# Kernel optimization log

Hardware: AMD Instinct MI355X
Metric: run time of the kernel (lower is better)

## Reference

```python
import jax, jax.numpy as jnp
import numpy as np
from functools import partial

K = 3
P = K * K * K          # 27 kernel points
G = 2                  # groups
PAD = 1
STRIDE = 1
DIL = 1
AXIS_SCALE = (0.5, 1.0, 1.0)   # (x, y, z) offset axis scale
CUR_SCALE = 0.5                # warmup scale at global_step=0
EPS = 1e-5


def setup_inputs() -> dict:
    key = jax.random.key(0)
    ks = jax.random.split(key, 8)
    C, OC = 64, 64
    N, D, H, W = 1, 32, 32, 32
    inp = {
        "x": jax.random.normal(ks[0], (N, C, D, H, W), jnp.float32),
        "dw_w": jax.random.normal(ks[1], (C, 1, K, K, K), jnp.float32) * 0.1,
        "gn_w": jnp.ones((C,), jnp.float32),
        "gn_b": jnp.zeros((C,), jnp.float32),
        "inp_w": jax.random.normal(ks[2], (C, C), jnp.float32) * (1.0 / np.sqrt(C)),
        "inp_b": jnp.zeros((C,), jnp.float32),
        # offset/mask weights are zero-init in the module; use small random values
        # so the deformable sampling path is exercised nontrivially.
        "off_w": jax.random.normal(ks[3], (C, G * P * 3), jnp.float32) * 0.01,
        "off_b": jnp.zeros((G * P * 3,), jnp.float32),
        "mask_w": jax.random.normal(ks[4], (C, G * P), jnp.float32) * 0.01,
        "mask_b": jnp.tile(jnp.full((P,), -5.0, jnp.float32).at[P // 2].set(0.0), (G,)),
        "out_w": jax.random.normal(ks[5], (C, OC), jnp.float32) * (1.0 / np.sqrt(C)),
        "out_b": jnp.zeros((OC,), jnp.float32),
    }
    return inp


def _trilinear(vol, loc):
    # vol: [Dp, Hp, Wp, gc]; loc: [..., 3] with (x, y, z) in [-1, 1]
    # grid_sample semantics: align_corners=False, padding_mode='zeros'
    Dp, Hp, Wp, _ = vol.shape
    ix = (loc[..., 0] + 1.0) * 0.5 * Wp - 0.5
    iy = (loc[..., 1] + 1.0) * 0.5 * Hp - 0.5
    iz = (loc[..., 2] + 1.0) * 0.5 * Dp - 0.5
    x0f, y0f, z0f = jnp.floor(ix), jnp.floor(iy), jnp.floor(iz)
    fx, fy, fz = ix - x0f, iy - y0f, iz - z0f
    x0, y0, z0 = x0f.astype(jnp.int32), y0f.astype(jnp.int32), z0f.astype(jnp.int32)
    out = jnp.zeros(loc.shape[:-1] + (vol.shape[-1],), vol.dtype)
    for dz in (0, 1):
        wz = fz if dz else 1.0 - fz
        cz = z0 + dz
        for dy in (0, 1):
            wy = fy if dy else 1.0 - fy
            cy = y0 + dy
            for dx in (0, 1):
                wx = fx if dx else 1.0 - fx
                cx = x0 + dx
                valid = ((cz >= 0) & (cz < Dp) & (cy >= 0) & (cy < Hp)
                         & (cx >= 0) & (cx < Wp))
                v = vol[jnp.clip(cz, 0, Dp - 1),
                        jnp.clip(cy, 0, Hp - 1),
                        jnp.clip(cx, 0, Wp - 1)]  # [..., gc]
                out = out + (wz * wy * wx * valid.astype(vol.dtype))[..., None] * v
    return out


def _forward(x, dw_w, gn_w, gn_b, inp_w, inp_b, off_w, off_b,
             mask_w, mask_b, out_w, out_b):
    N, C, D, H, W = x.shape
    gc = C // G
    # --- dw_conv: depthwise conv3d + GroupNorm(1, C) + GELU ---
    xc = jax.lax.conv_general_dilated(
        x, dw_w, window_strides=(1, 1, 1), padding=[(PAD, PAD)] * 3,
        dimension_numbers=("NCDHW", "OIDHW", "NCDHW"), feature_group_count=C)
    mu = xc.mean(axis=(1, 2, 3, 4), keepdims=True)
    var = ((xc - mu) ** 2).mean(axis=(1, 2, 3, 4), keepdims=True)
    xn = (xc - mu) * jax.lax.rsqrt(var + EPS)
    xn = xn * gn_w[None, :, None, None, None] + gn_b[None, :, None, None, None]
    x1 = jnp.transpose(jax.nn.gelu(xn), (0, 2, 3, 4, 1))       # [N,D,H,W,C]
    # --- offset / mask / input projection ---
    offset = x1 @ off_w + off_b                                  # [N,D,H,W,G*P*3]
    mask = jax.nn.softmax(
        (x1 @ mask_w + mask_b).reshape(N, D, H, W, G, P), axis=-1)
    xp = jnp.transpose(x, (0, 2, 3, 4, 1)) @ inp_w + inp_b       # [N,D,H,W,C]
    # --- core deformable sampling ---
    x_pad = jnp.pad(xp, ((0, 0), (PAD, PAD), (PAD, PAD), (PAD, PAD), (0, 0)))
    Dp, Hp, Wp = D + 2 * PAD, H + 2 * PAD, W + 2 * PAD
    Do = (D + 2 * PAD - DIL * (K - 1) - 1) // STRIDE + 1
    Ho = (H + 2 * PAD - DIL * (K - 1) - 1) // STRIDE + 1
    Wo = (W + 2 * PAD - DIL * (K - 1) - 1) // STRIDE + 1
    # reference grid (x/Wp, y/Hp, z/Dp)
    zc, yc, xc_ = jnp.meshgrid(jnp.arange(Do, dtype=jnp.float32),
                               jnp.arange(Ho, dtype=jnp.float32),
                               jnp.arange(Wo, dtype=jnp.float32), indexing="ij")
    ref = jnp.stack(((xc_ * STRIDE + PAD + 0.5) / Wp,
                     (yc * STRIDE + PAD + 0.5) / Hp,
                     (zc * STRIDE + PAD + 0.5) / Dp), axis=-1)   # [Do,Ho,Wo,3]
    # kernel grid
    lin = jnp.linspace(-(K - 1) // 2, (K - 1) // 2, K, dtype=jnp.float32)
    kz, ky, kx = jnp.meshgrid(lin, lin, lin, indexing="ij")
    kgrid = jnp.stack((kx * DIL / Wp, ky * DIL / Hp, kz * DIL / Dp),
                      axis=-1).reshape(P, 3)
    off = offset.reshape(N, Do, Ho, Wo, G, P, 3)
    off_norm = off / jnp.array([Wp, Hp, Dp], jnp.float32)
    axis = jnp.array(AXIS_SCALE, jnp.float32)
    loc = (ref[None, :, :, :, None, None, :]
           + kgrid[None, None, None, None, None, :, :]
           + off_norm * axis * CUR_SCALE)
    loc = loc * 2.0 - 1.0                                        # [N,Do,Ho,Wo,G,P,3]
    vol = jnp.transpose(x_pad.reshape(N, Dp, Hp, Wp, G, gc),
                        (0, 4, 1, 2, 3, 5))                      # [N,G,Dp,Hp,Wp,gc]
    locs = jnp.transpose(loc, (0, 4, 1, 2, 3, 5, 6))             # [N,G,Do,Ho,Wo,P,3]
    sampled = jax.vmap(jax.vmap(_trilinear))(vol, locs)          # [N,G,Do,Ho,Wo,P,gc]
    out = jnp.einsum("ngdhwpc,ndhwgp->ndhwgc", sampled, mask)
    out = out.reshape(N, Do, Ho, Wo, C)
    return out @ out_w + out_b                                   # [N,Do,Ho,Wo,OC]


def reference(x, dw_w, gn_w, gn_b, inp_w, inp_b, off_w, off_b,
              mask_w, mask_b, out_w, out_b):
    return _forward(x, dw_w, gn_w, gn_b, inp_w, inp_b, off_w, off_b,
                    mask_w, mask_b, out_w, out_b)
```

## Files before the change

kernel.cpp:

```cpp
#include <hip/hip_runtime.h>
#include <hip/hip_fp16.h>
#include <math.h>

#define SP 32768
#define PW 38
#define PW2 (PW*PW)
#define PVOX (PW*PW*PW)
#define OMS 228

typedef short bf16x8 __attribute__((ext_vector_type(8)));
typedef unsigned short u16x4 __attribute__((ext_vector_type(4)));
typedef float f32x4 __attribute__((ext_vector_type(4)));

__device__ __forceinline__ unsigned short f2b(float f) {
    unsigned u = __float_as_uint(f);
    u = (u + 0x7FFFu + ((u >> 16) & 1u)) >> 16;
    return (unsigned short)u;
}
__device__ __forceinline__ float b2f1(unsigned short s) {
    return __uint_as_float(((unsigned)s) << 16);
}
__device__ __forceinline__ __half2 h2(unsigned u) {
    return *reinterpret_cast<__half2*>(&u);
}
__device__ __forceinline__ int vox_of(int sb, int v) {
    int tw = sb & 7, th = (sb >> 3) & 15, td = sb >> 7;
    int vw = v & 3, vh = (v >> 2) & 1, vd = v >> 3;
    return (((td << 1) + vd) << 10) + (((th << 1) + vh) << 5) + (tw << 2) + vw;
}

__global__ void k_front(const float* __restrict__ x, const float* __restrict__ dw,
                        const float* __restrict__ off_w, const float* __restrict__ mask_w,
                        const float* __restrict__ off_b, const float* __restrict__ mask_b,
                        const float* __restrict__ inp_w, const float* __restrict__ inp_b,
                        const float* __restrict__ out_w,
                        unsigned short* __restrict__ WcatB, float* __restrict__ bcat,
                        unsigned short* __restrict__ outB,
                        unsigned short* __restrict__ xcb, float* __restrict__ partials,
                        unsigned short* __restrict__ xpad) {
    int bb = blockIdx.x, tid = threadIdx.x;
    if (bb < 72) {
        int idx = bb * 256 + tid;
        int j = idx >> 6, k = idx & 63;
        if (j < 224) {
            float v = 0.f;
            if (j < 162) v = off_w[k * 162 + j];
            else if (j < 216) v = mask_w[k * 54 + (j - 162)];
            WcatB[j * 64 + k] = f2b(v);
            if (k == 0) bcat[j] = (j < 162) ? off_b[j] : (j < 216 ? mask_b[j - 162] : 0.f);
        } else {
            outB[(j - 224) * 64 + k] = f2b(out_w[k * 64 + (j - 224)]);
        }
        return;
    }
    if (bb < 2120) {
        int b4 = bb - 72;
        int e4 = b4 * 256 + tid;
        int c = e4 >> 13, s4 = (e4 & 8191) << 2;
        int d = s4 >> 10, h = (s4 >> 5) & 31, w0 = s4 & 31;
        const float* xs = x + (size_t)c * SP;
        const float* wt = dw + c * 27;
        float a0 = 0.f, a1 = 0.f, a2 = 0.f, a3 = 0.f;
#pragma unroll
        for (int kd = 0; kd < 3; ++kd) {
            int zz = d + kd - 1; if ((unsigned)zz >= 32u) continue;
#pragma unroll
            for (int kh = 0; kh < 3; ++kh) {
                int yy = h + kh - 1; if ((unsigned)yy >= 32u) continue;
                const float* row = xs + (zz << 10) + (yy << 5) + w0;
                float4 L = *(const float4*)row;
                float xl = (w0 > 0) ? row[-1] : 0.f;
                float xr = (w0 < 28) ? row[4] : 0.f;
                const float* wr = wt + kd * 9 + kh * 3;
                float wm = wr[0], wc = wr[1], wp = wr[2];
                a0 = __builtin_fmaf(wm, xl,  __builtin_fmaf(wc, L.x, __builtin_fmaf(wp, L.y, a0)));
                a1 = __builtin_fmaf(wm, L.x, __builtin_fmaf(wc, L.y, __builtin_fmaf(wp, L.z, a1)));
                a2 = __builtin_fmaf(wm, L.y, __builtin_fmaf(wc, L.z, __builtin_fmaf(wp, L.w, a2)));
                a3 = __builtin_fmaf(wm, L.z, __builtin_fmaf(wc, L.w, __builtin_fmaf(wp, xr,  a3)));
            }
        }
        u16x4 o4; o4[0] = f2b(a0); o4[1] = f2b(a1); o4[2] = f2b(a2); o4[3] = f2b(a3);
        *(u16x4*)(xcb + (size_t)e4 * 4) = o4;
        float s1 = a0 + a1 + a2 + a3;
        float s2 = a0 * a0 + a1 * a1 + a2 * a2 + a3 * a3;
#pragma unroll
        for (int off = 32; off > 0; off >>= 1) {
            s1 += __shfl_xor(s1, off);
            s2 += __shfl_xor(s2, off);
        }
        __shared__ float ws[8];
        int wv = tid >> 6, lane = tid & 63;
        if (lane == 0) { ws[wv * 2] = s1; ws[wv * 2 + 1] = s2; }
        __syncthreads();
        if (tid == 0) {
            partials[b4 * 2 + 0] = ws[0] + ws[2] + ws[4] + ws[6];
            partials[b4 * 2 + 1] = ws[1] + ws[3] + ws[5] + ws[7];
        }
        return;
    }
    if (bb < 2632) {
        __shared__ unsigned short tileT[64][72];
        __shared__ unsigned short tileB[64][72];
        int s0b = (bb - 2120) * 64;
        int row = tid >> 6, lane = tid & 63;
        for (int c = row; c < 64; c += 4)
            tileT[lane][c] = f2b(x[(size_t)c * SP + s0b + lane]);
        {
            int n = tid & 63, k0 = (tid >> 6) * 16;
            u16x4 wb[4];
#pragma unroll
            for (int i = 0; i < 16; ++i)
                wb[i >> 2][i & 3] = f2b(inp_w[(size_t)(k0 + i) * 64 + n]);
#pragma unroll
            for (int q = 0; q < 4; ++q)
                *(u16x4*)(&tileB[n][k0 + q * 4]) = wb[q];
        }
        __syncthreads();
        int wv = row, quad = lane >> 4, col = lane & 15;
        int s0 = s0b + wv * 16;
        bf16x8 a0 = *(const bf16x8*)(&tileT[wv * 16 + col][quad * 8]);
        bf16x8 a1 = *(const bf16x8*)(&tileT[wv * 16 + col][32 + quad * 8]);
        int vp[4];
#pragma unroll
        for (int r = 0; r < 4; ++r) {
            int s = s0 + (quad << 2) + r;
            vp[r] = (((s >> 10) + 2) * PW + ((s >> 5) & 31) + 2) * PW + (s & 31) + 2;
        }
#pragma unroll
        for (int nt = 0; nt < 4; ++nt) {
            int n0 = nt * 16;
            bf16x8 b0 = *(const bf16x8*)(&tileB[n0 + col][quad * 8]);
            bf16x8 b1 = *(const bf16x8*)(&tileB[n0 + col][32 + quad * 8]);
            f32x4 c = {0.f, 0.f, 0.f, 0.f};
            c = __builtin_amdgcn_mfma_f32_16x16x32_bf16(a0, b0, c, 0, 0, 0);
            c = __builtin_amdgcn_mfma_f32_16x16x32_bf16(a1, b1, c, 0, 0, 0);
            float bq = inp_b[n0 + col];
#pragma unroll
            for (int r = 0; r < 4; ++r)
                xpad[(size_t)vp[r] * 64 + n0 + col] =
                    __half_as_ushort(__float2half(c[r] + bq));
        }
        return;
    }
    int cblk = bb - 2632;
    int j = tid >> 4, c4 = tid & 15;
    u16x4 z = {0, 0, 0, 0};
#pragma unroll
    for (int k = 0; k < 4; ++k) {
        int v = cblk * 64 + k * 16 + j;
        if (v >= PVOX) break;
        int zz = v / PW2, r = v - zz * PW2, yy = r / PW, xx = r - yy * PW;
        if (zz < 2 || zz > 33 || yy < 2 || yy > 33 || xx < 2 || xx > 33)
            *(u16x4*)(xpad + (size_t)v * 64 + c4 * 4) = z;
    }
}

template<int P0, int NP>
__device__ __forceinline__ void sampleN(const float* __restrict__ orow,
                                        const float* __restrict__ mrow,
                                        const char* __restrict__ volc,
                                        float xb, float yb, float zb,
                                        float* __restrict__ acc) {
#pragma unroll
    for (int i = 0; i < NP; ++i) {
        const int p = P0 + i;
        const int px = p % 3, py = (p / 3) % 3, pz = p / 9;
        float ox = orow[p * 3 + 0], oy = orow[p * 3 + 1], oz = orow[p * 3 + 2];
        float mk = mrow[p];
        float ix = __builtin_fmaf(0.25f, ox, xb + (float)px);
        float iy = __builtin_fmaf(0.5f, oy, yb + (float)py);
        float iz = __builtin_fmaf(0.5f, oz, zb + (float)pz);
        ix = fminf(fmaxf(ix, 0.f), 36.f);
        iy = fminf(fmaxf(iy, 0.f), 36.f);
        iz = fminf(fmaxf(iz, 0.f), 36.f);
        float xf = floorf(ix), yf = floorf(iy), zf = floorf(iz);
        float fx = ix - xf, fy = iy - yf, fz = iz - zf;
        float fi = __builtin_fmaf(zf, (float)PW2, __builtin_fmaf(yf, (float)PW, xf));
        int ib = ((int)fi) << 7;
        const char* base = volc + ib;
        uint4 r000 = *(const uint4*)(base);
        uint4 r001 = *(const uint4*)(base + 128);
        uint4 r010 = *(const uint4*)(base + PW * 128);
        uint4 r011 = *(const uint4*)(base + PW * 128 + 128);
        uint4 r100 = *(const uint4*)(base + PW2 * 128);
        uint4 r101 = *(const uint4*)(base + PW2 * 128 + 128);
        uint4 r110 = *(const uint4*)(base + (PW2 + PW) * 128);
        uint4 r111 = *(const uint4*)(base + (PW2 + PW) * 128 + 128);
        __half2 fx2 = __float2half2_rn(fx);
        __half2 fy2 = __float2half2_rn(fy);
        __half2 fz2 = __float2half2_rn(fz);
        #define TRI(comp, ci)                                                   \
        {                                                                       \
            __half2 t0 = __hfma2(fx2, __hsub2(h2(r001.comp), h2(r000.comp)), h2(r000.comp)); \
            __half2 t1 = __hfma2(fx2, __hsub2(h2(r011.comp), h2(r010.comp)), h2(r010.comp)); \
            __half2 t2 = __hfma2(fx2, __hsub2(h2(r101.comp), h2(r100.comp)), h2(r100.comp)); \
            __half2 t3 = __hfma2(fx2, __hsub2(h2(r111.comp), h2(r110.comp)), h2(r110.comp)); \
            __half2 u0 = __hfma2(fy2, __hsub2(t1, t0), t0);                     \
            __half2 u1 = __hfma2(fy2, __hsub2(t3, t2), t2);                     \
            __half2 rr = __hfma2(fz2, __hsub2(u1, u0), u0);                     \
            float2 ff = __half22float2(rr);                                     \
            acc[2 * ci + 0] = __builtin_fmaf(mk, ff.x, acc[2 * ci + 0]);        \
            acc[2 * ci + 1] = __builtin_fmaf(mk, ff.y, acc[2 * ci + 1]);        \
        }
        TRI(x, 0) TRI(y, 1) TRI(z, 2) TRI(w, 3)
        #undef TRI
    }
}

template<int P0, int NP>
__device__ __forceinline__ void sampleL(const float* __restrict__ orow,
                                        const float* __restrict__ mrow,
                                        const char* __restrict__ volp,
                                        float xb, float yb, float zb,
                                        float* __restrict__ acc) {
    float ox[NP], oy[NP], oz[NP], mk[NP];
#pragma unroll
    for (int i = 0; i < NP; ++i) {
        ox[i] = orow[(P0 + i) * 3 + 0];
        oy[i] = orow[(P0 + i) * 3 + 1];
        oz[i] = orow[(P0 + i) * 3 + 2];
        mk[i] = mrow[P0 + i];
    }
#pragma unroll
    for (int i = 0; i < NP; ++i) {
        const int p = P0 + i;
        const int px = p % 3, py = (p / 3) % 3, pz = p / 9;
        float ix = __builtin_fmaf(0.25f, ox[i], xb + (float)px);
        float iy = __builtin_fmaf(0.5f, oy[i], yb + (float)py);
        float iz = __builtin_fmaf(0.5f, oz[i], zb + (float)pz);
        ix = fminf(fmaxf(ix, 0.f), 6.999f);
        iy = fminf(fmaxf(iy, 0.f), 4.999f);
        iz = fminf(fmaxf(iz, 0.f), 4.999f);
        float xf = floorf(ix), yf = floorf(iy), zf = floorf(iz);
        float fx = ix - xf, fy = iy - yf, fz = iz - zf;
        float fi = __builtin_fmaf(zf, 48.f, __builtin_fmaf(yf, 8.f, xf));
        int rr = (int)fi;
        #define RD(o) (*(const uint4*)(volp + ((rr + (o)) << 7)))
        uint4 r000 = RD(0);
        uint4 r001 = RD(1);
        uint4 r010 = RD(8);
        uint4 r011 = RD(9);
        uint4 r100 = RD(48);
        uint4 r101 = RD(49);
        uint4 r110 = RD(56);
        uint4 r111 = RD(57);
        #undef RD
        __half2 fx2 = __float2half2_rn(fx);
        __half2 fy2 = __float2half2_rn(fy);
        __half2 fz2 = __float2half2_rn(fz);
        float m = mk[i];
        #define TRI(comp, ci)                                                   \
        {                                                                       \
            __half2 t0 = __hfma2(fx2, __hsub2(h2(r001.comp), h2(r000.comp)), h2(r000.comp)); \
            __half2 t1 = __hfma2(fx2, __hsub2(h2(r011.comp), h2(r010.comp)), h2(r010.comp)); \
            __half2 t2 = __hfma2(fx2, __hsub2(h2(r101.comp), h2(r100.comp)), h2(r100.comp)); \
            __half2 t3 = __hfma2(fx2, __hsub2(h2(r111.comp), h2(r110.comp)), h2(r110.comp)); \
            __half2 u0 = __hfma2(fy2, __hsub2(t1, t0), t0);                     \
            __half2 u1 = __hfma2(fy2, __hsub2(t3, t2), t2);                     \
            __half2 rr2 = __hfma2(fz2, __hsub2(u1, u0), u0);                    \
            float2 ff = __half22float2(rr2);                                    \
            acc[2 * ci + 0] = __builtin_fmaf(m, ff.x, acc[2 * ci + 0]);         \
            acc[2 * ci + 1] = __builtin_fmaf(m, ff.y, acc[2 * ci + 1]);         \
        }
        TRI(x, 0) TRI(y, 1) TRI(z, 2) TRI(w, 3)
        #undef TRI
    }
}

__global__ void __launch_bounds__(256, 2) k_main(const unsigned short* __restrict__ xcb,
                                                 const float* __restrict__ partials,
                                                 const float* __restrict__ gn_w,
                                                 const float* __restrict__ gn_b,
                                                 const unsigned short* __restrict__ xpad,
                                                 const unsigned short* __restrict__ WcatB,
                                                 const float* __restrict__ bcat,
                                                 const unsigned short* __restrict__ outB,
                                                 const float* __restrict__ out_b,
                                                 float* __restrict__ out) {
    __shared__ float om_s[16 * OMS];
    __shared__ unsigned short smb[16 * 72];
    __shared__ char vol[288 * 128];
    __shared__ float pbuf[16 * 64];
    __shared__ float gnw_s[64], gnb_s[64], ws[8];
    int tid = threadIdx.x, wv = tid >> 6, lane = tid & 63;
    int quad = lane >> 4, col = lane & 15;
    int sb = ((blockIdx.x & 7) << 8) | (blockIdx.x >> 3);
    int tw = sb & 7, th = (sb >> 3) & 15, td = sb >> 7;
    {
        const char* xp = (const char*)xpad;
#pragma unroll
        for (int k = 0; k < 3; ++k) {
            uint4 t[3];
#pragma unroll
            for (int j = 0; j < 3; ++j) {
                int u = tid + (k * 3 + j) * 256;
                int rr = u >> 3, ch = u & 7;
                int dz = rr / 48, rem = rr - dz * 48, dy = rem >> 3, dx = rem & 7;
                int pv = ((2 * td + dz) * PW + (2 * th + dy)) * PW + 4 * tw + dx;
                t[j] = *(const uint4*)(xp + ((size_t)pv << 7) + (ch << 4));
            }
#pragma unroll
            for (int j = 0; j < 3; ++j) {
                int u = tid + (k * 3 + j) * 256;
                *(uint4*)(vol + (u << 4)) = t[j];
            }
        }
    }
    {
        if (tid < 64) { gnw_s[tid] = gn_w[tid]; gnb_s[tid] = gn_b[tid]; }
        float a = 0.f, b = 0.f;
#pragma unroll
        for (int i = 0; i < 4; ++i) {
            float4 t = *(const float4*)(partials + 4 * (tid + i * 256));
            a += t.x + t.z;
            b += t.y + t.w;
        }
#pragma unroll
        for (int off = 32; off > 0; off >>= 1) {
            a += __shfl_xor(a, off);
            b += __shfl_xor(b, off);
        }
        if (lane == 0) { ws[wv * 2] = a; ws[wv * 2 + 1] = b; }
    }
    __syncthreads();
    const float Minv = 1.f / 2097152.f;
    float mu = (ws[0] + ws[2] + ws[4] + ws[6]) * Minv;
    float var = (ws[1] + ws[3] + ws[5] + ws[7]) * Minv - mu * mu;
    float rsq = rsqrtf(var + 1e-5f);
    {
        int v = tid >> 4, c0 = (tid & 15) * 4;
        int sv = vox_of(sb, v);
        u16x4 av;
#pragma unroll
        for (int i = 0; i < 4; ++i) {
            int c = c0 + i;
            float vx = (b2f1(xcb[(size_t)c * SP + sv]) - mu) * rsq * gnw_s[c] + gnb_s[c];
            float t2 = 1.5957691216057308f * (vx + 0.044715f * vx * vx * vx);
            av[i] = f2b(vx / (1.f + __expf(-t2)));
        }
        *(u16x4*)(&smb[v * 72 + c0]) = av;
    }
    __syncthreads();
    {
        bf16x8 a0 = *(const bf16x8*)(&smb[col * 72 + quad * 8]);
        bf16x8 a1 = *(const bf16x8*)(&smb[col * 72 + 32 + quad * 8]);
        for (int jt = wv; jt < 14; jt += 4) {
            int n0 = jt * 16;
            bf16x8 b0 = *(const bf16x8*)(WcatB + (n0 + col) * 64 + quad * 8);
            bf16x8 b1 = *(const bf16x8*)(WcatB + (n0 + col) * 64 + 32 + quad * 8);
            f32x4 c = {0.f, 0.f, 0.f, 0.f};
            c = __builtin_amdgcn_mfma_f32_16x16x32_bf16(a0, b0, c, 0, 0, 0);
            c = __builtin_amdgcn_mfma_f32_16x16x32_bf16(a1, b1, c, 0, 0, 0);
            float bb = bcat[n0 + col];
            int n = n0 + col, slot;
            if (n < 162) slot = n + ((n >= 81) ? 3 : 0);
            else { int n2 = n - 162; slot = 168 + n2 + ((n2 >= 27) ? 1 : 0); }
            if (n < 216) {
#pragma unroll
                for (int r = 0; r < 4; ++r)
                    om_s[(quad * 4 + r) * OMS + slot] = c[r] + bb;
            }
        }
    }
    __syncthreads();
    {
        int row = lane >> 2, sub = lane & 3;
        int vloc = (wv & 1) * 8 + (row >> 1), g = row & 1;
        float* m = &om_s[vloc * OMS + 168 + g * 28];
        float mv[7];
        float mx = -1e30f;
#pragma unroll
        for (int i = 0; i < 7; ++i) {
            int p = sub * 7 + i;
            mv[i] = (p < 27) ? m[p] : -1e30f;
            mx = fmaxf(mx, mv[i]);
        }
        mx = fmaxf(mx, __shfl_xor(mx, 1));
        mx = fmaxf(mx, __shfl_xor(mx, 2));
        float e[7], sm = 0.f;
#pragma unroll
        for (int i = 0; i < 7; ++i) { e[i] = __expf(mv[i] - mx); sm += e[i]; }
        sm += __shfl_xor(sm, 1);
        sm += __shfl_xor(sm, 2);
        float inv = 1.f / sm;
#pragma unroll
        for (int i = 0; i < 7; ++i) {
            int p = sub * 7 + i;
            if (p < 27) m[p] = e[i] * inv;
        }
    }
    {
        int half = wv & 1, mode = wv >> 1;
        int v = half * 8 + (lane >> 3);
        int oct = lane & 7, gg = oct >> 2;
        const float* orow = &om_s[v * OMS + gg * 84];
        const float* mrow = &om_s[v * OMS + 168 + gg * 28];
        float acc[8] = {0.f, 0.f, 0.f, 0.f, 0.f, 0.f, 0.f, 0.f};
        if (mode == 0) {
            int sv = vox_of(sb, v);
            float zb = (float)((sv >> 10) + 1);
            float yb = (float)(((sv >> 5) & 31) + 1);
            float xb = (float)((sv & 31) + 1);
            sampleN<0, 9>(orow, mrow, (const char*)xpad + oct * 16, xb, yb, zb, acc);
        } else {
            int vw = v & 3, vh = (v >> 2) & 1, vd = v >> 3;
            sampleL<9, 18>(orow, mrow, vol + oct * 16,
                           (float)(vw + 1), (float)(vh + 1), (float)(vd + 1), acc);
            float* pp = &pbuf[v * 64 + oct * 8];
            *(f32x4*)(pp) = *(f32x4*)(acc);
            *(f32x4*)(pp + 4) = *(f32x4*)(acc + 4);
        }
        __syncthreads();
        if (mode == 0) {
            const float* pp = &pbuf[v * 64 + oct * 8];
            bf16x8 sb8;
#pragma unroll
            for (int k = 0; k < 8; ++k) sb8[k] = (short)f2b(acc[k] + pp[k]);
            *(bf16x8*)(smb + v * 72 + oct * 8) = sb8;
        }
    }
    __syncthreads();
    {
        bf16x8 oa0 = *(const bf16x8*)(smb + col * 72 + quad * 8);
        bf16x8 oa1 = *(const bf16x8*)(smb + col * 72 + 32 + quad * 8);
        int n0 = wv * 16;
        bf16x8 b0 = *(const bf16x8*)(outB + (n0 + col) * 64 + quad * 8);
        bf16x8 b1 = *(const bf16x8*)(outB + (n0 + col) * 64 + 32 + quad * 8);
        f32x4 c = {0.f, 0.f, 0.f, 0.f};
        c = __builtin_amdgcn_mfma_f32_16x16x32_bf16(oa0, b0, c, 0, 0, 0);
        c = __builtin_amdgcn_mfma_f32_16x16x32_bf16(oa1, b1, c, 0, 0, 0);
        float bb = out_b[n0 + col];
        int vr[4];
#pragma unroll
        for (int r = 0; r < 4; ++r) vr[r] = vox_of(sb, quad * 4 + r);
#pragma unroll
        for (int r = 0; r < 4; ++r)
            out[(size_t)vr[r] * 64 + n0 + col] = c[r] + bb;
    }
}

extern "C" void kernel_launch(void* const* d_in, const int* in_sizes, int n_in,
                              void* d_out, int out_size, void* d_ws, size_t ws_size,
                              hipStream_t stream) {
    const float* x      = (const float*)d_in[0];
    const float* dw_w   = (const float*)d_in[1];
    const float* gn_w   = (const float*)d_in[2];
    const float* gn_b   = (const float*)d_in[3];
    const float* inp_w  = (const float*)d_in[4];
    const float* inp_b  = (const float*)d_in[5];
    const float* off_w  = (const float*)d_in[6];
    const float* off_b  = (const float*)d_in[7];
    const float* mask_w = (const float*)d_in[8];
    const float* mask_b = (const float*)d_in[9];
    const float* out_w  = (const float*)d_in[10];
    const float* out_b  = (const float*)d_in[11];

    char* B = (char*)d_ws;
    float*          partials = (float*)(B + 256);
    unsigned short* xcb      = (unsigned short*)(B + 65792);
    unsigned short* xpad     = (unsigned short*)(B + 16843008);
    unsigned short* WcatB    = (unsigned short*)(B + 30890240);
    float*          bcat     = (float*)(B + 30918912);
    unsigned short* outB     = (unsigned short*)(B + 30928128);
    float* out = (float*)d_out;

    k_front<<<72 + 2048 + 512 + 858, 256, 0, stream>>>(x, dw_w, off_w, mask_w, off_b, mask_b,
                                                       inp_w, inp_b, out_w, WcatB, bcat, outB,
                                                       xcb, partials, xpad);
    k_main<<<2048, 256, 0, stream>>>(xcb, partials, gn_w, gn_b, xpad,
                                     WcatB, bcat, outB, out_b, out);
}
```

Measured before the change: 145.2 us.

## Drop LDS volume staging; sample all points from global memory with balanced split

Result: no change. 144.4 us (-0.6%).

```diff
diff --git a/kernel.cpp b/kernel.cpp
--- a/kernel.cpp
+++ b/kernel.cpp
@@ -207,66 +207,6 @@
     }
 }
 
-template<int P0, int NP>
-__device__ __forceinline__ void sampleL(const float* __restrict__ orow,
-                                        const float* __restrict__ mrow,
-                                        const char* __restrict__ volp,
-                                        float xb, float yb, float zb,
-                                        float* __restrict__ acc) {
-    float ox[NP], oy[NP], oz[NP], mk[NP];
-#pragma unroll
-    for (int i = 0; i < NP; ++i) {
-        ox[i] = orow[(P0 + i) * 3 + 0];
-        oy[i] = orow[(P0 + i) * 3 + 1];
-        oz[i] = orow[(P0 + i) * 3 + 2];
-        mk[i] = mrow[P0 + i];
-    }
-#pragma unroll
-    for (int i = 0; i < NP; ++i) {
-        const int p = P0 + i;
-        const int px = p % 3, py = (p / 3) % 3, pz = p / 9;
-        float ix = __builtin_fmaf(0.25f, ox[i], xb + (float)px);
-        float iy = __builtin_fmaf(0.5f, oy[i], yb + (float)py);
-        float iz = __builtin_fmaf(0.5f, oz[i], zb + (float)pz);
-        ix = fminf(fmaxf(ix, 0.f), 6.999f);
-        iy = fminf(fmaxf(iy, 0.f), 4.999f);
-        iz = fminf(fmaxf(iz, 0.f), 4.999f);
-        float xf = floorf(ix), yf = floorf(iy), zf = floorf(iz);
-        float fx = ix - xf, fy = iy - yf, fz = iz - zf;
-        float fi = __builtin_fmaf(zf, 48.f, __builtin_fmaf(yf, 8.f, xf));
-        int rr = (int)fi;
-        #define RD(o) (*(const uint4*)(volp + ((rr + (o)) << 7)))
-        uint4 r000 = RD(0);
-        uint4 r001 = RD(1);
-        uint4 r010 = RD(8);
-        uint4 r011 = RD(9);
-        uint4 r100 = RD(48);
-        uint4 r101 = RD(49);
-        uint4 r110 = RD(56);
-        uint4 r111 = RD(57);
-        #undef RD
-        __half2 fx2 = __float2half2_rn(fx);
-        __half2 fy2 = __float2half2_rn(fy);
-        __half2 fz2 = __float2half2_rn(fz);
-        float m = mk[i];
-        #define TRI(comp, ci)                                                   \
-        {                                                                       \
-            __half2 t0 = __hfma2(fx2, __hsub2(h2(r001.comp), h2(r000.comp)), h2(r000.comp)); \
-            __half2 t1 = __hfma2(fx2, __hsub2(h2(r011.comp), h2(r010.comp)), h2(r010.comp)); \
-            __half2 t2 = __hfma2(fx2, __hsub2(h2(r101.comp), h2(r100.comp)), h2(r100.comp)); \
-            __half2 t3 = __hfma2(fx2, __hsub2(h2(r111.comp), h2(r110.comp)), h2(r110.comp)); \
-            __half2 u0 = __hfma2(fy2, __hsub2(t1, t0), t0);                     \
-            __half2 u1 = __hfma2(fy2, __hsub2(t3, t2), t2);                     \
-            __half2 rr2 = __hfma2(fz2, __hsub2(u1, u0), u0);                    \
-            float2 ff = __half22float2(rr2);                                    \
-            acc[2 * ci + 0] = __builtin_fmaf(m, ff.x, acc[2 * ci + 0]);         \
-            acc[2 * ci + 1] = __builtin_fmaf(m, ff.y, acc[2 * ci + 1]);         \
-        }
-        TRI(x, 0) TRI(y, 1) TRI(z, 2) TRI(w, 3)
-        #undef TRI
-    }
-}
-
 __global__ void __launch_bounds__(256, 2) k_main(const unsigned short* __restrict__ xcb,
                                                  const float* __restrict__ partials,
                                                  const float* __restrict__ gn_w,
@@ -279,33 +219,11 @@
                                                  float* __restrict__ out) {
     __shared__ float om_s[16 * OMS];
     __shared__ unsigned short smb[16 * 72];
-    __shared__ char vol[288 * 128];
     __shared__ float pbuf[16 * 64];
     __shared__ float gnw_s[64], gnb_s[64], ws[8];
     int tid = threadIdx.x, wv = tid >> 6, lane = tid & 63;
     int quad = lane >> 4, col = lane & 15;
     int sb = ((blockIdx.x & 7) << 8) | (blockIdx.x >> 3);
-    int tw = sb & 7, th = (sb >> 3) & 15, td = sb >> 7;
-    {
-        const char* xp = (const char*)xpad;
-#pragma unroll
-        for (int k = 0; k < 3; ++k) {
-            uint4 t[3];
-#pragma unroll
-            for (int j = 0; j < 3; ++j) {
-                int u = tid + (k * 3 + j) * 256;
-                int rr = u >> 3, ch = u & 7;
-                int dz = rr / 48, rem = rr - dz * 48, dy = rem >> 3, dx = rem & 7;
-                int pv = ((2 * td + dz) * PW + (2 * th + dy)) * PW + 4 * tw + dx;
-                t[j] = *(const uint4*)(xp + ((size_t)pv << 7) + (ch << 4));
-            }
-#pragma unroll
-            for (int j = 0; j < 3; ++j) {
-                int u = tid + (k * 3 + j) * 256;
-                *(uint4*)(vol + (u << 4)) = t[j];
-            }
-        }
-    }
     {
         if (tid < 64) { gnw_s[tid] = gn_w[tid]; gnb_s[tid] = gn_b[tid]; }
         float a = 0.f, b = 0.f;
@@ -364,54 +282,57 @@
     }
     __syncthreads();
     {
-        int row = lane >> 2, sub = lane & 3;
-        int vloc = (wv & 1) * 8 + (row >> 1), g = row & 1;
+        int row = wv * 8 + (lane >> 3);
+        int sub = lane & 7;
+        int vloc = row >> 1, g = row & 1;
         float* m = &om_s[vloc * OMS + 168 + g * 28];
-        float mv[7];
+        float mv[4];
         float mx = -1e30f;
 #pragma unroll
-        for (int i = 0; i < 7; ++i) {
-            int p = sub * 7 + i;
+        for (int i = 0; i < 4; ++i) {
+            int p = sub * 4 + i;
             mv[i] = (p < 27) ? m[p] : -1e30f;
             mx = fmaxf(mx, mv[i]);
         }
         mx = fmaxf(mx, __shfl_xor(mx, 1));
         mx = fmaxf(mx, __shfl_xor(mx, 2));
-        float e[7], sm = 0.f;
-#pragma unroll
-        for (int i = 0; i < 7; ++i) { e[i] = __expf(mv[i] - mx); sm += e[i]; }
+        mx = fmaxf(mx, __shfl_xor(mx, 4));
+        float e[4], sm = 0.f;
+#pragma unroll
+        for (int i = 0; i < 4; ++i) { e[i] = __expf(mv[i] - mx); sm += e[i]; }
         sm += __shfl_xor(sm, 1);
         sm += __shfl_xor(sm, 2);
+        sm += __shfl_xor(sm, 4);
         float inv = 1.f / sm;
 #pragma unroll
-        for (int i = 0; i < 7; ++i) {
-            int p = sub * 7 + i;
+        for (int i = 0; i < 4; ++i) {
+            int p = sub * 4 + i;
             if (p < 27) m[p] = e[i] * inv;
         }
     }
-    {
-        int half = wv & 1, mode = wv >> 1;
+    __syncthreads();
+    {
+        int half = wv & 1, ph = wv >> 1;
         int v = half * 8 + (lane >> 3);
         int oct = lane & 7, gg = oct >> 2;
         const float* orow = &om_s[v * OMS + gg * 84];
         const float* mrow = &om_s[v * OMS + 168 + gg * 28];
+        int sv = vox_of(sb, v);
+        float zb = (float)((sv >> 10) + 1);
+        float yb = (float)(((sv >> 5) & 31) + 1);
+        float xb = (float)((sv & 31) + 1);
+        const char* volc = (const char*)xpad + oct * 16;
         float acc[8] = {0.f, 0.f, 0.f, 0.f, 0.f, 0.f, 0.f, 0.f};
-        if (mode == 0) {
-            int sv = vox_of(sb, v);
-            float zb = (float)((sv >> 10) + 1);
-            float yb = (float)(((sv >> 5) & 31) + 1);
-            float xb = (float)((sv & 31) + 1);
-            sampleN<0, 9>(orow, mrow, (const char*)xpad + oct * 16, xb, yb, zb, acc);
+        if (ph == 0) {
+            sampleN<0, 14>(orow, mrow, volc, xb, yb, zb, acc);
         } else {
-            int vw = v & 3, vh = (v >> 2) & 1, vd = v >> 3;
-            sampleL<9, 18>(orow, mrow, vol + oct * 16,
-                           (float)(vw + 1), (float)(vh + 1), (float)(vd + 1), acc);
+            sampleN<14, 13>(orow, mrow, volc, xb, yb, zb, acc);
             float* pp = &pbuf[v * 64 + oct * 8];
             *(f32x4*)(pp) = *(f32x4*)(acc);
             *(f32x4*)(pp + 4) = *(f32x4*)(acc + 4);
         }
         __syncthreads();
-        if (mode == 0) {
+        if (ph == 0) {
             const float* pp = &pbuf[v * 64 + oct * 8];
             bf16x8 sb8;
 #pragma unroll
```
